# Performance work log

Measured on AMD Instinct MI355X. Metric: run time of the kernel, lower is better.

Reference implementation:

```python
import jax, jax.numpy as jnp
import numpy as np
import math

N_HEADS = 8
N_LEVELS = 3
N_POINTS = 4
D_MODEL = 128
D_HEAD = D_MODEL // N_HEADS  # 16
SHAPES = [(128, 128), (64, 64), (32, 32)]  # (H, W) per level
N = 1
LQ = 6400  # 80x80 BEV queries


def _xavier(k, shape):
    lim = math.sqrt(6.0 / (shape[0] + shape[1]))
    return jax.random.uniform(k, shape, jnp.float32, -lim, lim)


def _grid_init_bias():
    # faithful to _reset_parameters: per-head directional bias, scaled per point
    thetas = np.arange(N_HEADS, dtype=np.float32) * (2.0 * np.pi / N_HEADS)
    grid = np.stack([np.cos(thetas), np.sin(thetas)], -1)
    grid = grid / np.abs(grid).max(-1, keepdims=True)
    grid = np.tile(grid.reshape(N_HEADS, 1, 1, 2), (1, N_LEVELS, N_POINTS, 1))
    grid = grid * (np.arange(N_POINTS, dtype=np.float32) + 1.0).reshape(1, 1, N_POINTS, 1)
    return jnp.asarray(grid.reshape(-1), jnp.float32)


def setup_inputs() -> dict:
    key = jax.random.key(0)
    ks = jax.random.split(key, 12)
    query = jax.random.normal(ks[0], (N, LQ, D_MODEL), jnp.float32)
    reference_points = jax.random.uniform(ks[1], (N, LQ, N_LEVELS, 2), jnp.float32)
    feat0 = jax.random.normal(ks[2], (N, 128, SHAPES[0][0], SHAPES[0][1]), jnp.float32)
    feat1 = jax.random.normal(ks[3], (N, 128, SHAPES[1][0], SHAPES[1][1]), jnp.float32)
    feat2 = jax.random.normal(ks[4], (N, 64, SHAPES[2][0], SHAPES[2][1]), jnp.float32)
    input_spatial_shapes = jnp.array(SHAPES, jnp.int32)
    # torch inits weight to 0; use small random so grads wrt W_off are exercised
    W_off = jax.random.normal(ks[5], (N_HEADS * N_LEVELS * N_POINTS * 2, D_MODEL), jnp.float32) * 0.01
    b_off = _grid_init_bias()
    Wk0 = _xavier(ks[6], (128, 128)); bk0 = jnp.zeros((128,), jnp.float32)
    Wk1 = _xavier(ks[7], (128, 128)); bk1 = jnp.zeros((128,), jnp.float32)
    Wk2 = _xavier(ks[8], (128, 64)); bk2 = jnp.zeros((128,), jnp.float32)
    W_out = _xavier(ks[9], (128, 128)); b_out = jnp.zeros((128,), jnp.float32)
    return {
        'query': query, 'reference_points': reference_points,
        'feat0': feat0, 'feat1': feat1, 'feat2': feat2,
        'input_spatial_shapes': input_spatial_shapes,
        'W_off': W_off, 'b_off': b_off,
        'Wk0': Wk0, 'bk0': bk0, 'Wk1': Wk1, 'bk1': bk1, 'Wk2': Wk2, 'bk2': bk2,
        'W_out': W_out, 'b_out': b_out,
    }


def _bilinear_sample(feat, loc):
    # feat: (N, C, H, W); loc: (N, S, 2) in [0,1]; grid_sample align_corners=False, zero padding
    n, c, h, w = feat.shape
    x = loc[..., 0] * w - 0.5
    y = loc[..., 1] * h - 0.5
    x0 = jnp.floor(x); y0 = jnp.floor(y)
    wx = x - x0; wy = y - y0  # (N, S)
    x0i = x0.astype(jnp.int32); y0i = y0.astype(jnp.int32)
    flat = feat.reshape(n, c, h * w)

    def gather(xi, yi):
        valid = (xi >= 0) & (xi < w) & (yi >= 0) & (yi < h)
        idx = jnp.clip(yi, 0, h - 1) * w + jnp.clip(xi, 0, w - 1)
        v = jnp.take_along_axis(flat, idx[:, None, :], axis=2)  # (N, C, S)
        return v * valid[:, None, :].astype(feat.dtype)

    out = (gather(x0i, y0i) * ((1 - wx) * (1 - wy))[:, None, :]
           + gather(x0i + 1, y0i) * (wx * (1 - wy))[:, None, :]
           + gather(x0i, y0i + 1) * ((1 - wx) * wy)[:, None, :]
           + gather(x0i + 1, y0i + 1) * (wx * wy)[:, None, :])
    return out  # (N, C, S)


def _forward(query, reference_points, feat0, feat1, feat2, input_spatial_shapes,
             W_off, b_off, Wk0, bk0, Wk1, bk1, Wk2, bk2, W_out, b_out):
    n, lq, _ = query.shape
    off = (query @ W_off.T + b_off).reshape(n, lq, N_HEADS, N_LEVELS, N_POINTS, 2)
    shp = input_spatial_shapes.astype(query.dtype)
    norm = jnp.stack([shp[:, 1], shp[:, 0]], -1)  # (L, 2) = (W, H)
    # sampling locations in [0,1]: (N, Lq, H, L, P, 2)
    loc = reference_points[:, :, None, :, None, :] + off / norm[None, None, None, :, None, :]
    qh = query.reshape(n, lq, N_HEADS, D_HEAD)
    feats = [feat0, feat1, feat2]
    Wks = [Wk0, Wk1, Wk2]
    bks = [bk0, bk1, bk2]
    logits, vals = [], []
    for l in range(N_LEVELS):
        c = feats[l].shape[1]
        ll = loc[:, :, :, l, :, :].reshape(n, lq * N_HEADS * N_POINTS, 2)
        s = _bilinear_sample(feats[l], ll)  # (N, C, Lq*H*P)
        s = s.reshape(n, c, lq, N_HEADS, N_POINTS).transpose(0, 2, 3, 4, 1)  # (N, Lq, H, P, C)
        # per-head key projection: head h uses its 16-dim slice of the 128-d projection
        k = jnp.einsum('nqhpc,hdc->nqhpd', s, Wks[l].reshape(N_HEADS, D_HEAD, c))
        k = k + bks[l].reshape(N_HEADS, D_HEAD)[None, None, :, None, :]
        logits.append(jnp.einsum('nqhd,nqhpd->nqhp', qh, k))
        vals.append(k)
    logits = jnp.stack(logits, 3)  # (N, Lq, H, L, P)
    vals = jnp.stack(vals, 3)      # (N, Lq, H, L, P, D_HEAD)
    scale = 1.0 / math.sqrt(D_HEAD)
    attn = jax.nn.softmax((logits * scale).reshape(n, lq, N_HEADS, N_LEVELS * N_POINTS), -1)
    attn = attn.reshape(n, lq, N_HEADS, N_LEVELS, N_POINTS)
    out = jnp.einsum('nqhlp,nqhlpd->nqhd', attn, vals).reshape(n, lq, D_MODEL)
    out = out @ W_out.T + b_out
    return out.transpose(1, 0, 2)  # (Lq, N, C) per output.permute(1,0,2)


def reference(query, reference_points, feat0, feat1, feat2, input_spatial_shapes,
              W_off, b_off, Wk0, bk0, Wk1, bk1, Wk2, bk2, W_out, b_out):
    return _forward(query, reference_points, feat0, feat1, feat2, input_spatial_shapes,
                    W_off, b_off, Wk0, bk0, Wk1, bk1, Wk2, bk2, W_out, b_out)
```

## Files before the change

### kernel.cpp

```cpp
#include <hip/hip_runtime.h>
#include <hip/hip_bf16.h>
#include <math.h>

typedef __attribute__((ext_vector_type(8))) short bf16x8;
typedef __attribute__((ext_vector_type(4))) float f32x4;

__device__ __forceinline__ unsigned f2bfu(float f) {
    __hip_bfloat16 b = __float2bfloat16(f);
    return (unsigned)*reinterpret_cast<unsigned short*>(&b);
}

__device__ __forceinline__ bf16x8 cvt8(float4 a, float4 b) {
    bf16x8 r;
    r[0] = (short)f2bfu(a.x); r[1] = (short)f2bfu(a.y);
    r[2] = (short)f2bfu(a.z); r[3] = (short)f2bfu(a.w);
    r[4] = (short)f2bfu(b.x); r[5] = (short)f2bfu(b.y);
    r[6] = (short)f2bfu(b.z); r[7] = (short)f2bfu(b.w);
    return r;
}

template<int C>
__device__ __forceinline__ void proj_mfma(
    unsigned short* lds, const float* __restrict__ feat,
    const float* __restrict__ Wk, __hip_bfloat16* __restrict__ P,
    int HW, int pblk)
{
    constexpr int GR = C / 8;
    constexpr int KK = C / 32;
    const int tid = threadIdx.x;
    const int p0 = pblk * 128;

    for (int u = tid; u < (C / 2) * 32; u += 256) {
        int cip = u >> 5;
        int p4 = (u & 31) << 2;
        int ci = cip << 1;
        float4 lo = *reinterpret_cast<const float4*>(feat + (size_t)ci * HW + p0 + p4);
        float4 hi = *reinterpret_cast<const float4*>(feat + (size_t)(ci + 1) * HW + p0 + p4);
        float lov[4] = {lo.x, lo.y, lo.z, lo.w};
        float hiv[4] = {hi.x, hi.y, hi.z, hi.w};
        int g = ci >> 3;
        #pragma unroll
        for (int j = 0; j < 4; ++j) {
            int pix = p4 + j;
            int gs = g ^ (pix & (GR - 1));
            unsigned pack = f2bfu(lov[j]) | (f2bfu(hiv[j]) << 16);
            *reinterpret_cast<unsigned*>(lds + pix * C + gs * 8 + (ci & 7)) = pack;
        }
    }
    __syncthreads();

    const int wave = tid >> 6, lane = tid & 63;
    const int col = lane & 15, g4 = lane >> 4;

    bf16x8 bfrag[2][KK];
    #pragma unroll
    for (int st = 0; st < 2; ++st) {
        int pix = (wave * 2 + st) * 16 + col;
        #pragma unroll
        for (int kk = 0; kk < KK; ++kk) {
            int gs = (kk * 4 + g4) ^ (pix & (GR - 1));
            bfrag[st][kk] = *reinterpret_cast<const bf16x8*>(lds + pix * C + gs * 8);
        }
    }
    #pragma unroll
    for (int h = 0; h < 8; ++h) {
        bf16x8 afrag[KK];
        #pragma unroll
        for (int kk = 0; kk < KK; ++kk) {
            const float* wp = Wk + (size_t)(h * 16 + col) * C + kk * 32 + g4 * 8;
            afrag[kk] = cvt8(*reinterpret_cast<const float4*>(wp),
                             *reinterpret_cast<const float4*>(wp + 4));
        }
        #pragma unroll
        for (int st = 0; st < 2; ++st) {
            f32x4 acc = {0.f, 0.f, 0.f, 0.f};
            #pragma unroll
            for (int kk = 0; kk < KK; ++kk)
                acc = __builtin_amdgcn_mfma_f32_16x16x32_bf16(afrag[kk], bfrag[st][kk], acc, 0, 0, 0);
            int pix = p0 + (wave * 2 + st) * 16 + col;
            unsigned lo = f2bfu(acc[0]) | (f2bfu(acc[1]) << 16);
            unsigned hi = f2bfu(acc[2]) | (f2bfu(acc[3]) << 16);
            uint2 od = make_uint2(lo, hi);
            *reinterpret_cast<uint2*>(reinterpret_cast<char*>(P) +
                (size_t)(h * HW + pix) * 32 + g4 * 8) = od;
        }
    }
}

__device__ __forceinline__ void off_mfma(
    const float* __restrict__ query, const float* __restrict__ W_off,
    const float* __restrict__ b_off, float* __restrict__ offv, int qblk)
{
    const int tid = threadIdx.x;
    const int wave = tid >> 6, lane = tid & 63;
    const int col = lane & 15, g4 = lane >> 4;
    const int q = qblk * 64 + wave * 16 + col;

    bf16x8 bfrag[4];
    #pragma unroll
    for (int kk = 0; kk < 4; ++kk) {
        const float* qp = query + (size_t)q * 128 + kk * 32 + g4 * 8;
        bfrag[kk] = cvt8(*reinterpret_cast<const float4*>(qp),
                         *reinterpret_cast<const float4*>(qp + 4));
    }
    #pragma unroll
    for (int mt = 0; mt < 12; ++mt) {
        bf16x8 afrag[4];
        #pragma unroll
        for (int kk = 0; kk < 4; ++kk) {
            const float* wp = W_off + (size_t)(mt * 16 + col) * 128 + kk * 32 + g4 * 8;
            afrag[kk] = cvt8(*reinterpret_cast<const float4*>(wp),
                             *reinterpret_cast<const float4*>(wp + 4));
        }
        f32x4 acc = {0.f, 0.f, 0.f, 0.f};
        #pragma unroll
        for (int kk = 0; kk < 4; ++kk)
            acc = __builtin_amdgcn_mfma_f32_16x16x32_bf16(afrag[kk], bfrag[kk], acc, 0, 0, 0);
        float4 bias = *reinterpret_cast<const float4*>(b_off + mt * 16 + g4 * 4);
        float4 o = make_float4(acc[0] + bias.x, acc[1] + bias.y,
                               acc[2] + bias.z, acc[3] + bias.w);
        *reinterpret_cast<float4*>(offv + (size_t)q * 192 + mt * 16 + g4 * 4) = o;
    }
}

__global__ __launch_bounds__(256) void prep3_kernel(
    const float* __restrict__ feat0, const float* __restrict__ feat1,
    const float* __restrict__ feat2,
    const float* __restrict__ Wk0, const float* __restrict__ Wk1,
    const float* __restrict__ Wk2,
    __hip_bfloat16* __restrict__ P0, __hip_bfloat16* __restrict__ P1,
    __hip_bfloat16* __restrict__ P2,
    const float* __restrict__ query, const float* __restrict__ W_off,
    const float* __restrict__ b_off, float* __restrict__ offv)
{
    __shared__ __align__(16) unsigned short lds[128 * 128];
    int b = blockIdx.x;
    if (b < 128)      proj_mfma<128>(lds, feat0, Wk0, P0, 16384, b);
    else if (b < 160) proj_mfma<128>(lds, feat1, Wk1, P1, 4096, b - 128);
    else if (b < 168) proj_mfma<64>(lds, feat2, Wk2, P2, 1024, b - 160);
    else              off_mfma(query, W_off, b_off, offv, b - 168);
}

__global__ __launch_bounds__(128) void attn4_kernel(
    const float* __restrict__ query, const float* __restrict__ ref,
    const float* __restrict__ offv,
    const __hip_bfloat16* __restrict__ P0, const __hip_bfloat16* __restrict__ P1,
    const __hip_bfloat16* __restrict__ P2,
    const float* __restrict__ bk0, const float* __restrict__ bk1,
    const float* __restrict__ bk2,
    float* __restrict__ hout)
{
    __shared__ __align__(16) float q_sh[128];
    __shared__ __align__(16) float bias_sh[3][128];
    __shared__ float logit_sh[96];
    __shared__ __align__(16) float k_sh[96 * 20];
    __shared__ __align__(16) unsigned gaddr[96][4];
    __shared__ __align__(16) float gw[96][4];
    int q = blockIdx.x;
    int tid = threadIdx.x;
    q_sh[tid] = query[q * 128 + tid];
    bias_sh[0][tid] = bk0[tid];
    bias_sh[1][tid] = bk1[tid];
    bias_sh[2][tid] = bk2[tid];
    if (tid < 96) {
        int s = tid;
        int h = (s * 171) >> 11;
        int lp = s - h * 12;
        int l = lp >> 2;
        int W = 128 >> l;
        float ox = offv[q * 192 + 2 * s];
        float oy = offv[q * 192 + 2 * s + 1];
        float x = fmaf(ref[q * 6 + 2 * l], (float)W, ox) - 0.5f;
        float y = fmaf(ref[q * 6 + 2 * l + 1], (float)W, oy) - 0.5f;
        float x0f = floorf(x), y0f = floorf(y);
        float wx = x - x0f, wy = y - y0f;
        int x0 = (int)x0f, y0 = (int)y0f;
        int x1 = x0 + 1, y1 = y0 + 1;
        float mx0 = (x0 >= 0 && x0 < W) ? 1.f : 0.f;
        float mx1 = (x1 >= 0 && x1 < W) ? 1.f : 0.f;
        float my0 = (y0 >= 0 && y0 < W) ? 1.f : 0.f;
        float my1 = (y1 >= 0 && y1 < W) ? 1.f : 0.f;
        int xc0 = min(max(x0, 0), W - 1), xc1 = min(max(x1, 0), W - 1);
        int yc0 = min(max(y0, 0), W - 1), yc1 = min(max(y1, 0), W - 1);
        unsigned pb = (unsigned)(h * W * W) * 32u;
        gaddr[s][0] = pb + (unsigned)(yc0 * W + xc0) * 32u;
        gaddr[s][1] = pb + (unsigned)(yc0 * W + xc1) * 32u;
        gaddr[s][2] = pb + (unsigned)(yc1 * W + xc0) * 32u;
        gaddr[s][3] = pb + (unsigned)(yc1 * W + xc1) * 32u;
        gw[s][0] = (1.f - wx) * (1.f - wy) * mx0 * my0;
        gw[s][1] = wx * (1.f - wy) * mx1 * my0;
        gw[s][2] = (1.f - wx) * wy * mx0 * my1;
        gw[s][3] = wx * wy * mx1 * my1;
    }
    __syncthreads();

    const int quad = tid & 3;
    uint2 raw[3][4];
    float4 wv[3];
    int hs[3], lps[3], lvs[3];
    #pragma unroll
    for (int it = 0; it < 3; ++it) {
        int s = it * 32 + (tid >> 2);
        int h = (s * 171) >> 11;
        int lp = s - h * 12;
        int l = lp >> 2;
        hs[it] = h; lps[it] = lp; lvs[it] = l;
        uint4 av = *reinterpret_cast<const uint4*>(&gaddr[s][0]);
        wv[it] = *reinterpret_cast<const float4*>(&gw[s][0]);
        const char* base = ((l == 0) ? (const char*)P0 :
                            (l == 1) ? (const char*)P1 : (const char*)P2) + quad * 8;
        raw[it][0] = *reinterpret_cast<const uint2*>(base + av.x);
        raw[it][1] = *reinterpret_cast<const uint2*>(base + av.y);
        raw[it][2] = *reinterpret_cast<const uint2*>(base + av.z);
        raw[it][3] = *reinterpret_cast<const uint2*>(base + av.w);
    }
    #pragma unroll
    for (int it = 0; it < 3; ++it) {
        int s = it * 32 + (tid >> 2);
        int h = hs[it], l = lvs[it];
        float k0 = 0.f, k1 = 0.f, k2 = 0.f, k3 = 0.f;
        float wc[4] = {wv[it].x, wv[it].y, wv[it].z, wv[it].w};
        #pragma unroll
        for (int cnr = 0; cnr < 4; ++cnr) {
            unsigned a = raw[it][cnr].x, b2 = raw[it][cnr].y;
            float w = wc[cnr];
            k0 = fmaf(w, __uint_as_float(a << 16), k0);
            k1 = fmaf(w, __uint_as_float(a & 0xffff0000u), k1);
            k2 = fmaf(w, __uint_as_float(b2 << 16), k2);
            k3 = fmaf(w, __uint_as_float(b2 & 0xffff0000u), k3);
        }
        int co = h * 16 + quad * 4;
        float4 bias = *reinterpret_cast<const float4*>(&bias_sh[l][co]);
        k0 += bias.x; k1 += bias.y; k2 += bias.z; k3 += bias.w;
        float4 qv = *reinterpret_cast<const float4*>(&q_sh[co]);
        float lg = k0 * qv.x;
        lg = fmaf(k1, qv.y, lg);
        lg = fmaf(k2, qv.z, lg);
        lg = fmaf(k3, qv.w, lg);
        lg += __shfl_xor(lg, 1);
        lg += __shfl_xor(lg, 2);
        *reinterpret_cast<float4*>(&k_sh[s * 20 + quad * 4]) = make_float4(k0, k1, k2, k3);
        if (quad == 0) logit_sh[s] = lg;
    }
    __syncthreads();

    int h2 = tid >> 4, dd = tid & 15;
    float m = -1e30f;
    #pragma unroll
    for (int j = 0; j < 12; ++j) m = fmaxf(m, logit_sh[h2 * 12 + j]);
    float ssum = 0.f, o = 0.f;
    #pragma unroll
    for (int j = 0; j < 12; ++j) {
        float e = __expf(0.25f * (logit_sh[h2 * 12 + j] - m));
        ssum += e;
        o = fmaf(e, k_sh[(h2 * 12 + j) * 20 + dd], o);
    }
    hout[q * 128 + tid] = o / ssum;
}

__global__ __launch_bounds__(256) void outp2_kernel(
    const float* __restrict__ hin, const float* __restrict__ W_out,
    const float* __restrict__ b_out, float* __restrict__ out)
{
    __shared__ __align__(16) float w_sh[64 * 128];
    __shared__ __align__(16) float q_sh[64 * 128];
    int b = blockIdx.x;
    int qblk = b >> 1;
    int half = b & 1;
    int rbase = half * 64;
    int q0 = qblk * 64;
    int tid = threadIdx.x;

    for (int idx = tid; idx < 64 * 32; idx += 256) {
        int rl = idx >> 5;
        int ci4 = idx & 31;
        float4 v = *reinterpret_cast<const float4*>(&W_out[(rbase + rl) * 128 + ci4 * 4]);
        *reinterpret_cast<float4*>(&w_sh[rl * 128 + ((ci4 ^ (rl & 31)) << 2)]) = v;
    }
    for (int idx = tid; idx < 64 * 32; idx += 256) {
        int qq = idx >> 5;
        int ci4 = idx & 31;
        *reinterpret_cast<float4*>(&q_sh[qq * 128 + ci4 * 4]) =
            *reinterpret_cast<const float4*>(&hin[(q0 + qq) * 128 + ci4 * 4]);
    }
    __syncthreads();

    int c0 = tid & 31;
    int qg = tid >> 5;
    float acc[2][8];
    #pragma unroll
    for (int k = 0; k < 2; ++k)
        #pragma unroll
        for (int j = 0; j < 8; ++j) acc[k][j] = 0.f;

    #pragma unroll 4
    for (int ci4 = 0; ci4 < 32; ++ci4) {
        float4 A0 = *reinterpret_cast<const float4*>(&w_sh[c0 * 128 + ((ci4 ^ c0) << 2)]);
        float4 A1 = *reinterpret_cast<const float4*>(&w_sh[(c0 + 32) * 128 + ((ci4 ^ c0) << 2)]);
        #pragma unroll
        for (int j = 0; j < 8; ++j) {
            float4 B = *reinterpret_cast<const float4*>(&q_sh[(qg * 8 + j) * 128 + ci4 * 4]);
            acc[0][j] = fmaf(A0.x, B.x, acc[0][j]);
            acc[0][j] = fmaf(A0.y, B.y, acc[0][j]);
            acc[0][j] = fmaf(A0.z, B.z, acc[0][j]);
            acc[0][j] = fmaf(A0.w, B.w, acc[0][j]);
            acc[1][j] = fmaf(A1.x, B.x, acc[1][j]);
            acc[1][j] = fmaf(A1.y, B.y, acc[1][j]);
            acc[1][j] = fmaf(A1.z, B.z, acc[1][j]);
            acc[1][j] = fmaf(A1.w, B.w, acc[1][j]);
        }
    }
    #pragma unroll
    for (int k = 0; k < 2; ++k) {
        int r = rbase + c0 + 32 * k;
        float bias = b_out[r];
        #pragma unroll
        for (int j = 0; j < 8; ++j)
            out[(q0 + qg * 8 + j) * 128 + r] = acc[k][j] + bias;
    }
}

extern "C" void kernel_launch(void* const* d_in, const int* in_sizes, int n_in,
                              void* d_out, int out_size, void* d_ws, size_t ws_size,
                              hipStream_t stream) {
    const float* query = (const float*)d_in[0];
    const float* ref   = (const float*)d_in[1];
    const float* feat0 = (const float*)d_in[2];
    const float* feat1 = (const float*)d_in[3];
    const float* feat2 = (const float*)d_in[4];
    const float* W_off = (const float*)d_in[6];
    const float* b_off = (const float*)d_in[7];
    const float* Wk0   = (const float*)d_in[8];
    const float* bk0   = (const float*)d_in[9];
    const float* Wk1   = (const float*)d_in[10];
    const float* bk1   = (const float*)d_in[11];
    const float* Wk2   = (const float*)d_in[12];
    const float* bk2   = (const float*)d_in[13];
    const float* W_out = (const float*)d_in[14];
    const float* b_out = (const float*)d_in[15];
    float* out = (float*)d_out;

    __hip_bfloat16* P0 = (__hip_bfloat16*)d_ws;
    __hip_bfloat16* P1 = P0 + 8 * 16384 * 16;
    __hip_bfloat16* P2 = P1 + 8 * 4096 * 16;
    float* offv = (float*)(P2 + 8 * 1024 * 16);
    float* hout = offv + 6400 * 192;

    hipLaunchKernelGGL(prep3_kernel, dim3(268), dim3(256), 0, stream,
                       feat0, feat1, feat2, Wk0, Wk1, Wk2, P0, P1, P2,
                       query, W_off, b_off, offv);
    hipLaunchKernelGGL(attn4_kernel, dim3(6400), dim3(128), 0, stream,
                       query, ref, offv, P0, P1, P2, bk0, bk1, bk2, hout);
    hipLaunchKernelGGL(outp2_kernel, dim3(200), dim3(256), 0, stream,
                       hout, W_out, b_out, out);
}
```

Before: 133.5 us.

## Fuse output projection into attention kernel, two queries per block

Removes the separate output-projection kernel by having each attention block compute its 128-d head output in LDS and then multiply it by a transposed W_out read from global memory. The transpose is done by one extra block in the prep kernel. Each attention block now handles two queries with 256 threads, so there are fewer blocks. This drops one launch and the hout round-trip through global memory. In exchange, every block re-reads the full 64 KB W_out from cache, with serial per-thread FMAs instead of a tiled GEMM.

```diff
diff --git a/kernel.cpp b/kernel.cpp
--- a/kernel.cpp
+++ b/kernel.cpp
@@ -123,7 +123,7 @@
     }
 }
 
-__global__ __launch_bounds__(256) void prep3_kernel(
+__global__ __launch_bounds__(256) void prep4_kernel(
     const float* __restrict__ feat0, const float* __restrict__ feat1,
     const float* __restrict__ feat2,
     const float* __restrict__ Wk0, const float* __restrict__ Wk1,
@@ -131,47 +131,63 @@
     __hip_bfloat16* __restrict__ P0, __hip_bfloat16* __restrict__ P1,
     __hip_bfloat16* __restrict__ P2,
     const float* __restrict__ query, const float* __restrict__ W_off,
-    const float* __restrict__ b_off, float* __restrict__ offv)
+    const float* __restrict__ b_off, float* __restrict__ offv,
+    const float* __restrict__ W_out, float* __restrict__ WT)
 {
     __shared__ __align__(16) unsigned short lds[128 * 128];
     int b = blockIdx.x;
     if (b < 128)      proj_mfma<128>(lds, feat0, Wk0, P0, 16384, b);
     else if (b < 160) proj_mfma<128>(lds, feat1, Wk1, P1, 4096, b - 128);
     else if (b < 168) proj_mfma<64>(lds, feat2, Wk2, P2, 1024, b - 160);
-    else              off_mfma(query, W_off, b_off, offv, b - 168);
-}
-
-__global__ __launch_bounds__(128) void attn4_kernel(
+    else if (b < 268) off_mfma(query, W_off, b_off, offv, b - 168);
+    else {
+        for (int idx = threadIdx.x; idx < 128 * 128; idx += 256) {
+            int co = idx >> 7, ci = idx & 127;
+            WT[ci * 128 + co] = W_out[co * 128 + ci];
+        }
+    }
+}
+
+__global__ __launch_bounds__(256) void attn5_kernel(
     const float* __restrict__ query, const float* __restrict__ ref,
     const float* __restrict__ offv,
     const __hip_bfloat16* __restrict__ P0, const __hip_bfloat16* __restrict__ P1,
     const __hip_bfloat16* __restrict__ P2,
     const float* __restrict__ bk0, const float* __restrict__ bk1,
     const float* __restrict__ bk2,
-    float* __restrict__ hout)
+    const float* __restrict__ WT, const float* __restrict__ b_out,
+    float* __restrict__ out)
 {
-    __shared__ __align__(16) float q_sh[128];
+    __shared__ __align__(16) float q_sh[2][128];
     __shared__ __align__(16) float bias_sh[3][128];
-    __shared__ float logit_sh[96];
-    __shared__ __align__(16) float k_sh[96 * 20];
-    __shared__ __align__(16) unsigned gaddr[96][4];
-    __shared__ __align__(16) float gw[96][4];
-    int q = blockIdx.x;
-    int tid = threadIdx.x;
-    q_sh[tid] = query[q * 128 + tid];
-    bias_sh[0][tid] = bk0[tid];
-    bias_sh[1][tid] = bk1[tid];
-    bias_sh[2][tid] = bk2[tid];
-    if (tid < 96) {
-        int s = tid;
+    __shared__ float logit_sh[2][96];
+    __shared__ __align__(16) float k_sh[2][96 * 20];
+    __shared__ __align__(16) unsigned gaddr[2][96][4];
+    __shared__ __align__(16) float gw[2][96][4];
+    __shared__ __align__(16) float h_sh[2][128];
+    const int q0 = blockIdx.x * 2;
+    const int tid = threadIdx.x;
+    const int qloc = tid >> 7;
+    const int t = tid & 127;
+
+    q_sh[qloc][t] = query[(q0 + qloc) * 128 + t];
+    if (tid < 128) {
+        bias_sh[0][t] = bk0[t];
+        bias_sh[1][t] = bk1[t];
+        bias_sh[2][t] = bk2[t];
+    }
+    if (tid < 192) {
+        int qg = tid / 96;
+        int s = tid - qg * 96;
+        int qq = q0 + qg;
         int h = (s * 171) >> 11;
         int lp = s - h * 12;
         int l = lp >> 2;
         int W = 128 >> l;
-        float ox = offv[q * 192 + 2 * s];
-        float oy = offv[q * 192 + 2 * s + 1];
-        float x = fmaf(ref[q * 6 + 2 * l], (float)W, ox) - 0.5f;
-        float y = fmaf(ref[q * 6 + 2 * l + 1], (float)W, oy) - 0.5f;
+        float ox = offv[qq * 192 + 2 * s];
+        float oy = offv[qq * 192 + 2 * s + 1];
+        float x = fmaf(ref[qq * 6 + 2 * l], (float)W, ox) - 0.5f;
+        float y = fmaf(ref[qq * 6 + 2 * l + 1], (float)W, oy) - 0.5f;
         float x0f = floorf(x), y0f = floorf(y);
         float wx = x - x0f, wy = y - y0f;
         int x0 = (int)x0f, y0 = (int)y0f;
@@ -183,30 +199,30 @@
         int xc0 = min(max(x0, 0), W - 1), xc1 = min(max(x1, 0), W - 1);
         int yc0 = min(max(y0, 0), W - 1), yc1 = min(max(y1, 0), W - 1);
         unsigned pb = (unsigned)(h * W * W) * 32u;
-        gaddr[s][0] = pb + (unsigned)(yc0 * W + xc0) * 32u;
-        gaddr[s][1] = pb + (unsigned)(yc0 * W + xc1) * 32u;
-        gaddr[s][2] = pb + (unsigned)(yc1 * W + xc0) * 32u;
-        gaddr[s][3] = pb + (unsigned)(yc1 * W + xc1) * 32u;
-        gw[s][0] = (1.f - wx) * (1.f - wy) * mx0 * my0;
-        gw[s][1] = wx * (1.f - wy) * mx1 * my0;
-        gw[s][2] = (1.f - wx) * wy * mx0 * my1;
-        gw[s][3] = wx * wy * mx1 * my1;
+        gaddr[qg][s][0] = pb + (unsigned)(yc0 * W + xc0) * 32u;
+        gaddr[qg][s][1] = pb + (unsigned)(yc0 * W + xc1) * 32u;
+        gaddr[qg][s][2] = pb + (unsigned)(yc1 * W + xc0) * 32u;
+        gaddr[qg][s][3] = pb + (unsigned)(yc1 * W + xc1) * 32u;
+        gw[qg][s][0] = (1.f - wx) * (1.f - wy) * mx0 * my0;
+        gw[qg][s][1] = wx * (1.f - wy) * mx1 * my0;
+        gw[qg][s][2] = (1.f - wx) * wy * mx0 * my1;
+        gw[qg][s][3] = wx * wy * mx1 * my1;
     }
     __syncthreads();
 
     const int quad = tid & 3;
     uint2 raw[3][4];
     float4 wv[3];
-    int hs[3], lps[3], lvs[3];
     #pragma unroll
     for (int it = 0; it < 3; ++it) {
-        int s = it * 32 + (tid >> 2);
+        int sg = it * 64 + (tid >> 2);
+        int qg = (sg >= 96) ? 1 : 0;
+        int s = sg - qg * 96;
         int h = (s * 171) >> 11;
         int lp = s - h * 12;
         int l = lp >> 2;
-        hs[it] = h; lps[it] = lp; lvs[it] = l;
-        uint4 av = *reinterpret_cast<const uint4*>(&gaddr[s][0]);
-        wv[it] = *reinterpret_cast<const float4*>(&gw[s][0]);
+        uint4 av = *reinterpret_cast<const uint4*>(&gaddr[qg][s][0]);
+        wv[it] = *reinterpret_cast<const float4*>(&gw[qg][s][0]);
         const char* base = ((l == 0) ? (const char*)P0 :
                             (l == 1) ? (const char*)P1 : (const char*)P2) + quad * 8;
         raw[it][0] = *reinterpret_cast<const uint2*>(base + av.x);
@@ -216,8 +232,12 @@
     }
     #pragma unroll
     for (int it = 0; it < 3; ++it) {
-        int s = it * 32 + (tid >> 2);
-        int h = hs[it], l = lvs[it];
+        int sg = it * 64 + (tid >> 2);
+        int qg = (sg >= 96) ? 1 : 0;
+        int s = sg - qg * 96;
+        int h = (s * 171) >> 11;
+        int lp = s - h * 12;
+        int l = lp >> 2;
         float k0 = 0.f, k1 = 0.f, k2 = 0.f, k3 = 0.f;
         float wc[4] = {wv[it].x, wv[it].y, wv[it].z, wv[it].w};
         #pragma unroll
@@ -232,91 +252,48 @@
         int co = h * 16 + quad * 4;
         float4 bias = *reinterpret_cast<const float4*>(&bias_sh[l][co]);
         k0 += bias.x; k1 += bias.y; k2 += bias.z; k3 += bias.w;
-        float4 qv = *reinterpret_cast<const float4*>(&q_sh[co]);
+        float4 qv = *reinterpret_cast<const float4*>(&q_sh[qg][co]);
         float lg = k0 * qv.x;
         lg = fmaf(k1, qv.y, lg);
         lg = fmaf(k2, qv.z, lg);
         lg = fmaf(k3, qv.w, lg);
         lg += __shfl_xor(lg, 1);
         lg += __shfl_xor(lg, 2);
-        *reinterpret_cast<float4*>(&k_sh[s * 20 + quad * 4]) = make_float4(k0, k1, k2, k3);
-        if (quad == 0) logit_sh[s] = lg;
+        *reinterpret_cast<float4*>(&k_sh[qg][s * 20 + quad * 4]) = make_float4(k0, k1, k2, k3);
+        if (quad == 0) logit_sh[qg][s] = lg;
     }
     __syncthreads();
 
-    int h2 = tid >> 4, dd = tid & 15;
-    float m = -1e30f;
-    #pragma unroll
-    for (int j = 0; j < 12; ++j) m = fmaxf(m, logit_sh[h2 * 12 + j]);
-    float ssum = 0.f, o = 0.f;
-    #pragma unroll
-    for (int j = 0; j < 12; ++j) {
-        float e = __expf(0.25f * (logit_sh[h2 * 12 + j] - m));
-        ssum += e;
-        o = fmaf(e, k_sh[(h2 * 12 + j) * 20 + dd], o);
-    }
-    hout[q * 128 + tid] = o / ssum;
-}
-
-__global__ __launch_bounds__(256) void outp2_kernel(
-    const float* __restrict__ hin, const float* __restrict__ W_out,
-    const float* __restrict__ b_out, float* __restrict__ out)
-{
-    __shared__ __align__(16) float w_sh[64 * 128];
-    __shared__ __align__(16) float q_sh[64 * 128];
-    int b = blockIdx.x;
-    int qblk = b >> 1;
-    int half = b & 1;
-    int rbase = half * 64;
-    int q0 = qblk * 64;
-    int tid = threadIdx.x;
-
-    for (int idx = tid; idx < 64 * 32; idx += 256) {
-        int rl = idx >> 5;
-        int ci4 = idx & 31;
-        float4 v = *reinterpret_cast<const float4*>(&W_out[(rbase + rl) * 128 + ci4 * 4]);
-        *reinterpret_cast<float4*>(&w_sh[rl * 128 + ((ci4 ^ (rl & 31)) << 2)]) = v;
-    }
-    for (int idx = tid; idx < 64 * 32; idx += 256) {
-        int qq = idx >> 5;
-        int ci4 = idx & 31;
-        *reinterpret_cast<float4*>(&q_sh[qq * 128 + ci4 * 4]) =
-            *reinterpret_cast<const float4*>(&hin[(q0 + qq) * 128 + ci4 * 4]);
+    {
+        int qg = tid >> 7;
+        int h2 = (tid >> 4) & 7;
+        int dd = tid & 15;
+        float m = -1e30f;
+        #pragma unroll
+        for (int j = 0; j < 12; ++j) m = fmaxf(m, logit_sh[qg][h2 * 12 + j]);
+        float ssum = 0.f, o = 0.f;
+        #pragma unroll
+        for (int j = 0; j < 12; ++j) {
+            float e = __expf(0.25f * (logit_sh[qg][h2 * 12 + j] - m));
+            ssum += e;
+            o = fmaf(e, k_sh[qg][(h2 * 12 + j) * 20 + dd], o);
+        }
+        h_sh[qg][h2 * 16 + dd] = o / ssum;
     }
     __syncthreads();
 
-    int c0 = tid & 31;
-    int qg = tid >> 5;
-    float acc[2][8];
-    #pragma unroll
-    for (int k = 0; k < 2; ++k)
-        #pragma unroll
-        for (int j = 0; j < 8; ++j) acc[k][j] = 0.f;
-
-    #pragma unroll 4
-    for (int ci4 = 0; ci4 < 32; ++ci4) {
-        float4 A0 = *reinterpret_cast<const float4*>(&w_sh[c0 * 128 + ((ci4 ^ c0) << 2)]);
-        float4 A1 = *reinterpret_cast<const float4*>(&w_sh[(c0 + 32) * 128 + ((ci4 ^ c0) << 2)]);
-        #pragma unroll
-        for (int j = 0; j < 8; ++j) {
-            float4 B = *reinterpret_cast<const float4*>(&q_sh[(qg * 8 + j) * 128 + ci4 * 4]);
-            acc[0][j] = fmaf(A0.x, B.x, acc[0][j]);
-            acc[0][j] = fmaf(A0.y, B.y, acc[0][j]);
-            acc[0][j] = fmaf(A0.z, B.z, acc[0][j]);
-            acc[0][j] = fmaf(A0.w, B.w, acc[0][j]);
-            acc[1][j] = fmaf(A1.x, B.x, acc[1][j]);
-            acc[1][j] = fmaf(A1.y, B.y, acc[1][j]);
-            acc[1][j] = fmaf(A1.z, B.z, acc[1][j]);
-            acc[1][j] = fmaf(A1.w, B.w, acc[1][j]);
-        }
-    }
-    #pragma unroll
-    for (int k = 0; k < 2; ++k) {
-        int r = rbase + c0 + 32 * k;
-        float bias = b_out[r];
-        #pragma unroll
-        for (int j = 0; j < 8; ++j)
-            out[(q0 + qg * 8 + j) * 128 + r] = acc[k][j] + bias;
+    {
+        const float* wt = WT + t;
+        float acc = 0.f;
+        #pragma unroll 8
+        for (int k = 0; k < 128; k += 4) {
+            float4 h4 = *reinterpret_cast<const float4*>(&h_sh[qloc][k]);
+            acc = fmaf(wt[(k + 0) * 128], h4.x, acc);
+            acc = fmaf(wt[(k + 1) * 128], h4.y, acc);
+            acc = fmaf(wt[(k + 2) * 128], h4.z, acc);
+            acc = fmaf(wt[(k + 3) * 128], h4.w, acc);
+        }
+        out[(q0 + qloc) * 128 + t] = acc + b_out[t];
     }
 }
 
@@ -344,13 +321,12 @@
     __hip_bfloat16* P1 = P0 + 8 * 16384 * 16;
     __hip_bfloat16* P2 = P1 + 8 * 4096 * 16;
     float* offv = (float*)(P2 + 8 * 1024 * 16);
-    float* hout = offv + 6400 * 192;
-
-    hipLaunchKernelGGL(prep3_kernel, dim3(268), dim3(256), 0, stream,
+    float* WT   = offv + 6400 * 192;
+
+    hipLaunchKernelGGL(prep4_kernel, dim3(269), dim3(256), 0, stream,
                        feat0, feat1, feat2, Wk0, Wk1, Wk2, P0, P1, P2,
-                       query, W_off, b_off, offv);
-    hipLaunchKernelGGL(attn4_kernel, dim3(6400), dim3(128), 0, stream,
-                       query, ref, offv, P0, P1, P2, bk0, bk1, bk2, hout);
-    hipLaunchKernelGGL(outp2_kernel, dim3(200), dim3(256), 0, stream,
-                       hout, W_out, b_out, out);
-}
+                       query, W_off, b_off, offv, W_out, WT);
+    hipLaunchKernelGGL(attn5_kernel, dim3(3200), dim3(256), 0, stream,
+                       query, ref, offv, P0, P1, P2, bk0, bk1, bk2,
+                       WT, b_out, out);
+}
```

After: 138.7 us. 1.04x slower.
